# Optimization experiments

Measured on AMD Instinct MI355X. Metric: run time of the kernel, lower is better.

The kernel has to match this reference:

```python
import jax, jax.numpy as jnp
import numpy as np

N_NODES = 100000
N_EDGES = 3200000
IN_F, HID, N_CLS = 512, 16, 7


def setup_inputs() -> dict:
    key = jax.random.key(0)
    k1, k2, k3, k4 = jax.random.split(key, 4)
    x = jax.random.normal(k1, (N_NODES, IN_F), dtype=jnp.float32)
    edge_index = jax.random.randint(k2, (2, N_EDGES), 0, N_NODES, dtype=jnp.int32)
    W1 = jax.random.normal(k3, (IN_F, HID), dtype=jnp.float32) * (1.0 / np.sqrt(IN_F))
    b1 = jnp.zeros((HID,), dtype=jnp.float32)
    W2 = jax.random.normal(k4, (HID, N_CLS), dtype=jnp.float32) * (1.0 / np.sqrt(HID))
    b2 = jnp.zeros((N_CLS,), dtype=jnp.float32)
    return {"x": x, "edge_index": edge_index, "W1": W1, "b1": b1, "W2": W2, "b2": b2}


def _gcn_norm(src, dst, n_nodes):
    # symmetric normalization with self-loops already included in (src, dst)
    deg = jax.ops.segment_sum(jnp.ones(dst.shape, jnp.float32), dst, num_segments=n_nodes)
    dinv = jnp.where(deg > 0, jax.lax.rsqrt(deg), 0.0)
    return dinv[src] * dinv[dst]  # [E]


def _gcn_conv(h, src, dst, norm, W, b, n_nodes):
    # transform-first (PyG GCNConv), then normalized scatter-add aggregation
    h = h @ W                                   # [N, out]
    msg = h[src] * norm[:, None]                # gather + scale, [E, out]
    out = jax.ops.segment_sum(msg, dst, num_segments=n_nodes)  # scatter-add
    return out + b


def reference(x, edge_index, W1, b1, W2, b2):
    n = x.shape[0]
    loops = jnp.arange(n, dtype=edge_index.dtype)
    src = jnp.concatenate([edge_index[0], loops])
    dst = jnp.concatenate([edge_index[1], loops])
    norm = _gcn_norm(src, dst, n)
    h = _gcn_conv(x, src, dst, norm, W1, b1, n)
    h = jax.nn.relu(h)
    out = _gcn_conv(h, src, dst, norm, W2, b2, n)
    return out
```

## Files before the change

### kernel.cpp

```cpp
#include <hip/hip_runtime.h>

#define CHUNK 8192
#define BMAX 512

typedef __attribute__((address_space(3))) unsigned int lds_u32;
typedef const __attribute__((address_space(1))) unsigned int glb_u32;

__device__ __forceinline__ void gload16(const float* g, float* l) {
    __builtin_amdgcn_global_load_lds((glb_u32*)g, (lds_u32*)l, 16, 0, 0);
}


__global__ __launch_bounds__(256) void k_coarse_hist(const int* __restrict__ dst, int E,
                                                     int* __restrict__ bc,
                                                     int* __restrict__ blockBase, int B) {
    __shared__ int cnt[BMAX];
    int t = threadIdx.x;
    cnt[t] = 0; cnt[t + 256] = 0;
    __syncthreads();
    int e0 = blockIdx.x * CHUNK;
#pragma unroll
    for (int it = 0; it < CHUNK / 256; ++it) {
        int e = e0 + it * 256 + t;
        if (e < E) atomicAdd(&cnt[dst[e] >> 8], 1);
    }
    __syncthreads();
    for (int b = t; b < B; b += 256) {
        int c = cnt[b];
        if (c > 0) blockBase[(size_t)blockIdx.x * B + b] = atomicAdd(&bc[b], c);
    }
}

__global__ void k_scan_bsums(int* bsums, int nb) {
    __shared__ int s[2][512];
    int t = threadIdx.x;
    int v = (t < nb) ? bsums[t] : 0;
    int p = 0;
    s[0][t] = v;
    __syncthreads();
    for (int off = 1; off < 512; off <<= 1) {
        s[p ^ 1][t] = s[p][t] + ((t >= off) ? s[p][t - off] : 0);
        p ^= 1;
        __syncthreads();
    }
    if (t < nb) bsums[t] = s[p][t] - v;
}


__global__ __launch_bounds__(256) void k_coarse_scatter(const int* __restrict__ src,
                                                        const int* __restrict__ dst, int E,
                                                        const int* __restrict__ bucketBase,
                                                        const int* __restrict__ blockBase, int B,
                                                        unsigned int* __restrict__ ebuf) {
    __shared__ int run[BMAX];
    int t = threadIdx.x;
    run[t] = 0; run[t + 256] = 0;
    __syncthreads();
    int e0 = blockIdx.x * CHUNK;
#pragma unroll
    for (int it = 0; it < CHUNK / 256; ++it) {
        int e = e0 + it * 256 + t;
        if (e < E) {
            int d = dst[e];
            int b = d >> 8;
            int rank = atomicAdd(&run[b], 1);
            int pos = bucketBase[b] + blockBase[(size_t)blockIdx.x * B + b] + rank;
            ebuf[pos] = ((unsigned int)(d & 255) << 24) | (unsigned int)src[e];
        }
    }
}


__global__ __launch_bounds__(256) void k_bucket_hist(const unsigned int* __restrict__ ebuf,
                                                     const int* __restrict__ bucketBase,
                                                     int E, int N, int B,
                                                     int* __restrict__ hist,
                                                     float* __restrict__ dinv) {
    __shared__ int cnt[256];
    int t = threadIdx.x;
    int b = blockIdx.x;
    cnt[t] = 0;
    __syncthreads();
    int e0 = bucketBase[b];
    int e1 = (b + 1 < B) ? bucketBase[b + 1] : E;
    for (int e = e0 + t; e < e1; e += 256) atomicAdd(&cnt[ebuf[e] >> 24], 1);
    __syncthreads();
    int node = b * 256 + t;
    if (node < N) {
        hist[node] = cnt[t];
        dinv[node] = rsqrtf((float)(cnt[t] + 1));
    }
}


__global__ __launch_bounds__(256) void k_fine_scatter(const unsigned int* __restrict__ ebuf,
                                                      const int* __restrict__ bucketBase,
                                                      const int* __restrict__ hist,
                                                      int E, int N, int B,
                                                      int* __restrict__ rowStart,
                                                      int* __restrict__ csr_src) {
    __shared__ int s[2][256];
    __shared__ int cnt[256];
    int t = threadIdx.x;
    int b = blockIdx.x;
    int node = b * 256 + t;
    int v = (node < N) ? hist[node] : 0;
    int p = 0;
    s[0][t] = v;
    __syncthreads();
    for (int off = 1; off < 256; off <<= 1) {
        s[p ^ 1][t] = s[p][t] + ((t >= off) ? s[p][t - off] : 0);
        p ^= 1;
        __syncthreads();
    }
    int rs = bucketBase[b] + s[p][t] - v;
    if (node < N) rowStart[node] = rs;
    cnt[t] = rs;
    __syncthreads();
    int e0 = bucketBase[b];
    int e1 = (b + 1 < B) ? bucketBase[b + 1] : E;
    for (int e = e0 + t; e < e1; e += 256) {
        unsigned int w = ebuf[e];
        int pos = atomicAdd(&cnt[w >> 24], 1);
        csr_src[pos] = (int)(w & 0xFFFFFFu);
    }
}


__global__ __launch_bounds__(256) void k_gemm1(const float* __restrict__ x,
                                               const float* __restrict__ W1,
                                               const float* __restrict__ dinv,
                                               int N, float* __restrict__ h1) {
    __shared__ float xs[2][256 * 32];
    const int t = threadIdx.x;
    const int R0 = blockIdx.x * 256;
    const int tk = t & 7;

    const float* gbase[8];
#pragma unroll
    for (int it = 0; it < 8; ++it) {
        int r = it * 32 + (t >> 3);
        int j4 = tk ^ (r & 7);
        int row = R0 + r;
        if (row >= N) row = N - 1;
        gbase[it] = x + (size_t)row * 512 + j4 * 4;
    }

    float acc[16];
#pragma unroll
    for (int c = 0; c < 16; ++c) acc[c] = 0.0f;

#pragma unroll
    for (int it = 0; it < 8; ++it)
        gload16(gbase[it], &xs[0][(it * 256 + t) * 4]);
    __syncthreads();

    int p = 0;
    for (int ch = 0; ch < 16; ++ch) {
        if (ch + 1 < 16) {
#pragma unroll
            for (int it = 0; it < 8; ++it)
                gload16(gbase[it] + (ch + 1) * 32, &xs[p ^ 1][(it * 256 + t) * 4]);
        }
        const float* xr = &xs[p][t * 32];
#pragma unroll
        for (int j4 = 0; j4 < 8; ++j4) {
            float4 xv = *(const float4*)(xr + ((j4 ^ tk) << 2));
            float xe[4] = {xv.x, xv.y, xv.z, xv.w};
            int k = ch * 32 + j4 * 4;
#pragma unroll
            for (int d = 0; d < 4; ++d) {
                const float* w = W1 + (k + d) * 16;
#pragma unroll
                for (int c = 0; c < 16; ++c) acc[c] = fmaf(xe[d], w[c], acc[c]);
            }
        }
        __syncthreads();
        p ^= 1;
    }

    int row = R0 + t;
    if (row < N) {
        float di = dinv[row];
#pragma unroll
        for (int c = 0; c < 16; ++c) acc[c] *= di;
        float4* o = (float4*)(h1 + (size_t)row * 16);
        o[0] = make_float4(acc[0], acc[1], acc[2], acc[3]);
        o[1] = make_float4(acc[4], acc[5], acc[6], acc[7]);
        o[2] = make_float4(acc[8], acc[9], acc[10], acc[11]);
        o[3] = make_float4(acc[12], acc[13], acc[14], acc[15]);
    }
}


__global__ void k_gather1(const float* __restrict__ h1, const int* __restrict__ csr_src,
                          const int* __restrict__ rowStart, const int* __restrict__ hist,
                          const float* __restrict__ dinv, const float* __restrict__ b1,
                          int N, float* __restrict__ relu1) {
    int g = blockIdx.x * blockDim.x + threadIdx.x;
    int i = g >> 4, c = g & 15;
    if (i >= N) return;
    float ssum = h1[(size_t)i * 16 + c];
    int e0 = rowStart[i], e1 = e0 + hist[i];
    for (int e = e0; e < e1; ++e) {
        int s = csr_src[e];
        ssum += h1[(size_t)s * 16 + c];
    }
    float v = fmaf(dinv[i], ssum, b1[c]);
    relu1[(size_t)i * 16 + c] = fmaxf(v, 0.0f);
}


__global__ void k_h2(const float* __restrict__ relu1, const float* __restrict__ W2,
                     const float* __restrict__ dinv, int N, float* __restrict__ h2) {
    int i = blockIdx.x * blockDim.x + threadIdx.x;
    if (i >= N) return;
    float r[16];
#pragma unroll
    for (int q = 0; q < 4; ++q) {
        float4 v = *(const float4*)(relu1 + (size_t)i * 16 + q * 4);
        r[q * 4 + 0] = v.x; r[q * 4 + 1] = v.y; r[q * 4 + 2] = v.z; r[q * 4 + 3] = v.w;
    }
    float di = dinv[i];
#pragma unroll
    for (int c2 = 0; c2 < 7; ++c2) {
        float a = 0.0f;
#pragma unroll
        for (int c = 0; c < 16; ++c) a = fmaf(r[c], W2[c * 7 + c2], a);
        h2[(size_t)i * 7 + c2] = a * di;
    }
}


__global__ void k_gather2(const float* __restrict__ h2, const int* __restrict__ csr_src,
                          const int* __restrict__ rowStart, const int* __restrict__ hist,
                          const float* __restrict__ dinv, const float* __restrict__ b2,
                          int N, float* __restrict__ out) {
    int g = blockIdx.x * blockDim.x + threadIdx.x;
    int i = g >> 3, c = g & 7;
    if (i >= N || c >= 7) return;
    float ssum = h2[(size_t)i * 7 + c];
    int e0 = rowStart[i], e1 = e0 + hist[i];
    for (int e = e0; e < e1; ++e) {
        int s = csr_src[e];
        ssum += h2[(size_t)s * 7 + c];
    }
    out[(size_t)i * 7 + c] = fmaf(dinv[i], ssum, b2[c]);
}


extern "C" void kernel_launch(void* const* d_in, const int* in_sizes, int n_in,
                              void* d_out, int out_size, void* d_ws, size_t ws_size,
                              hipStream_t stream) {
    const float* x  = (const float*)d_in[0];
    const int*   ei = (const int*)d_in[1];
    const float* W1 = (const float*)d_in[2];
    const float* b1 = (const float*)d_in[3];
    const float* W2 = (const float*)d_in[4];
    const float* b2 = (const float*)d_in[5];
    float* out = (float*)d_out;

    const int N = in_sizes[0] / 512;
    const int E = in_sizes[1] / 2;
    const int* src = ei;
    const int* dst = ei + E;

    const int nb  = (N + 255) / 256;
    const int B   = nb;
    const int nbA = (E + CHUNK - 1) / CHUNK;

    char* ws = (char*)d_ws;
    auto alloc = [&](size_t bytes) {
        char* p = ws;
        ws += (bytes + 511) & ~(size_t)511;
        return p;
    };
    int*   hist      = (int*)alloc((size_t)N * 4);
    float* dinv      = (float*)alloc((size_t)N * 4);
    int*   rowStart  = (int*)alloc((size_t)N * 4);
    int*   bc        = (int*)alloc((size_t)(B + 1) * 4);
    int*   blockBase = (int*)alloc((size_t)nbA * B * 4);
    int*   csr_src   = (int*)alloc((size_t)E * 4);
    size_t featBytes = (size_t)N * 16 * 4 * 2 + (size_t)N * 7 * 4;
    size_t ebufBytes = (size_t)E * 4;
    char* regB = alloc(featBytes > ebufBytes ? featBytes : ebufBytes);
    unsigned int* ebuf = (unsigned int*)regB;
    float* h1    = (float*)regB;
    float* relu1 = h1 + (size_t)N * 16;
    float* h2    = relu1 + (size_t)N * 16;

    hipMemsetAsync(bc, 0, (size_t)B * 4, stream);
    k_coarse_hist<<<nbA, 256, 0, stream>>>(dst, E, bc, blockBase, B);
    k_scan_bsums<<<1, 512, 0, stream>>>(bc, B);
    k_coarse_scatter<<<nbA, 256, 0, stream>>>(src, dst, E, bc, blockBase, B, ebuf);
    k_bucket_hist<<<B, 256, 0, stream>>>(ebuf, bc, E, N, B, hist, dinv);
    k_fine_scatter<<<B, 256, 0, stream>>>(ebuf, bc, hist, E, N, B, rowStart, csr_src);
    k_gemm1<<<nb, 256, 0, stream>>>(x, W1, dinv, N, h1);
    k_gather1<<<(N * 16 + 255) / 256, 256, 0, stream>>>(h1, csr_src, rowStart, hist, dinv, b1, N, relu1);
    k_h2<<<nb, 256, 0, stream>>>(relu1, W2, dinv, N, h2);
    k_gather2<<<(N * 8 + 255) / 256, 256, 0, stream>>>(h2, csr_src, rowStart, hist, dinv, b2, N, out);
}
```

Before: 582.6 us.

## Split GEMM1 K-dimension across waves with LDS reduction, 64 rows per block

Rewrites the first-layer GEMM so each block handles 64 rows instead of 256. The whole 64x512 tile is loaded into LDS at once, and each of the four waves computes partial sums over a quarter of K. The partials are then reduced through LDS before dinv scaling and the store. This launches four times more blocks to raise parallelism and occupancy across CUs and removes the chunked double-buffer loop. In exchange it gives up copy/compute overlap within a block, uses 128KB LDS per block (likely one block per CU), and adds a reduction step.

Measured after the change: 604.4 us. +3.8%, slower.

```diff
diff --git a/kernel.cpp b/kernel.cpp
--- a/kernel.cpp
+++ b/kernel.cpp
@@ -131,64 +131,63 @@
                                                const float* __restrict__ W1,
                                                const float* __restrict__ dinv,
                                                int N, float* __restrict__ h1) {
-    __shared__ float xs[2][256 * 32];
+    __shared__ float xs[64 * 512];
     const int t = threadIdx.x;
-    const int R0 = blockIdx.x * 256;
-    const int tk = t & 7;
-
-    const float* gbase[8];
-#pragma unroll
-    for (int it = 0; it < 8; ++it) {
-        int r = it * 32 + (t >> 3);
-        int j4 = tk ^ (r & 7);
+    const int lane = t & 63;
+    const int w = __builtin_amdgcn_readfirstlane(t >> 6);
+    const int R0 = blockIdx.x * 64;
+
+#pragma unroll
+    for (int u = 0; u < 32; ++u) {
+        int r = w * 16 + (u >> 1);
+        int h = u & 1;
         int row = R0 + r;
         if (row >= N) row = N - 1;
-        gbase[it] = x + (size_t)row * 512 + j4 * 4;
-    }
+        const float* src = x + (size_t)row * 512 + h * 256 + ((lane ^ (r & 7)) << 2);
+        gload16(src, &xs[r * 512 + h * 256]);
+    }
+    __syncthreads();
 
     float acc[16];
 #pragma unroll
     for (int c = 0; c < 16; ++c) acc[c] = 0.0f;
-
-#pragma unroll
-    for (int it = 0; it < 8; ++it)
-        gload16(gbase[it], &xs[0][(it * 256 + t) * 4]);
-    __syncthreads();
-
-    int p = 0;
-    for (int ch = 0; ch < 16; ++ch) {
-        if (ch + 1 < 16) {
-#pragma unroll
-            for (int it = 0; it < 8; ++it)
-                gload16(gbase[it] + (ch + 1) * 32, &xs[p ^ 1][(it * 256 + t) * 4]);
+    const int sw = lane & 7;
+#pragma unroll 4
+    for (int k4 = 0; k4 < 32; ++k4) {
+        int g = w * 32 + k4;
+        const float4 xv = *(const float4*)&xs[lane * 512 + ((g ^ sw) << 2)];
+        float xe[4] = {xv.x, xv.y, xv.z, xv.w};
+        int k = g << 2;
+#pragma unroll
+        for (int d = 0; d < 4; ++d) {
+            const float* wp = W1 + (k + d) * 16;
+#pragma unroll
+            for (int c = 0; c < 16; ++c) acc[c] = fmaf(xe[d], wp[c], acc[c]);
         }
-        const float* xr = &xs[p][t * 32];
-#pragma unroll
-        for (int j4 = 0; j4 < 8; ++j4) {
-            float4 xv = *(const float4*)(xr + ((j4 ^ tk) << 2));
-            float xe[4] = {xv.x, xv.y, xv.z, xv.w};
-            int k = ch * 32 + j4 * 4;
-#pragma unroll
-            for (int d = 0; d < 4; ++d) {
-                const float* w = W1 + (k + d) * 16;
-#pragma unroll
-                for (int c = 0; c < 16; ++c) acc[c] = fmaf(xe[d], w[c], acc[c]);
-            }
-        }
-        __syncthreads();
-        p ^= 1;
-    }
-
-    int row = R0 + t;
+    }
+    __syncthreads();
+
+    float* red = xs;
+#pragma unroll
+    for (int cg = 0; cg < 4; ++cg)
+        *(float4*)&red[(w * 64 + lane) * 16 + cg * 4] =
+            make_float4(acc[cg * 4], acc[cg * 4 + 1], acc[cg * 4 + 2], acc[cg * 4 + 3]);
+    __syncthreads();
+
+    int r = t >> 2, cg = (t & 3) * 4;
+    int row = R0 + r;
     if (row < N) {
+        float4 s0 = *(float4*)&red[(0 * 64 + r) * 16 + cg];
+        float4 s1 = *(float4*)&red[(1 * 64 + r) * 16 + cg];
+        float4 s2 = *(float4*)&red[(2 * 64 + r) * 16 + cg];
+        float4 s3 = *(float4*)&red[(3 * 64 + r) * 16 + cg];
         float di = dinv[row];
-#pragma unroll
-        for (int c = 0; c < 16; ++c) acc[c] *= di;
-        float4* o = (float4*)(h1 + (size_t)row * 16);
-        o[0] = make_float4(acc[0], acc[1], acc[2], acc[3]);
-        o[1] = make_float4(acc[4], acc[5], acc[6], acc[7]);
-        o[2] = make_float4(acc[8], acc[9], acc[10], acc[11]);
-        o[3] = make_float4(acc[12], acc[13], acc[14], acc[15]);
+        float4 o;
+        o.x = (s0.x + s1.x + s2.x + s3.x) * di;
+        o.y = (s0.y + s1.y + s2.y + s3.y) * di;
+        o.z = (s0.z + s1.z + s2.z + s3.z) * di;
+        o.w = (s0.w + s1.w + s2.w + s3.w) * di;
+        *(float4*)(h1 + (size_t)row * 16 + cg) = o;
     }
 }
 
@@ -268,6 +267,7 @@
     const int nb  = (N + 255) / 256;
     const int B   = nb;
     const int nbA = (E + CHUNK - 1) / CHUNK;
+    const int nb64 = (N + 63) / 64;
 
     char* ws = (char*)d_ws;
     auto alloc = [&](size_t bytes) {
@@ -295,7 +295,7 @@
     k_coarse_scatter<<<nbA, 256, 0, stream>>>(src, dst, E, bc, blockBase, B, ebuf);
     k_bucket_hist<<<B, 256, 0, stream>>>(ebuf, bc, E, N, B, hist, dinv);
     k_fine_scatter<<<B, 256, 0, stream>>>(ebuf, bc, hist, E, N, B, rowStart, csr_src);
-    k_gemm1<<<nb, 256, 0, stream>>>(x, W1, dinv, N, h1);
+    k_gemm1<<<nb64, 256, 0, stream>>>(x, W1, dinv, N, h1);
     k_gather1<<<(N * 16 + 255) / 256, 256, 0, stream>>>(h1, csr_src, rowStart, hist, dinv, b1, N, relu1);
     k_h2<<<nb, 256, 0, stream>>>(relu1, W2, dinv, N, h2);
     k_gather2<<<(N * 8 + 255) / 256, 256, 0, stream>>>(h2, csr_src, rowStart, hist, dinv, b2, N, out);
```

## Split gemm1 output columns across waves with 64-row blocks for occupancy

Applied to the files above, without the earlier changes.

The first-layer GEMM now processes 64 rows per block instead of 256. Each of the four waves computes a 4-column slice of the 16 outputs for all 64 rows, so a thread holds 4 accumulators instead of 16. LDS shrinks from 64KB to 16KB, and launch bounds request 6 blocks per CU, with the aim of more occupancy and more blocks to hide the latency of streaming x. In exchange, each x element in LDS is read by four waves instead of one, and W1 is read four times per row.

New measurement: 558.7 us. -4.1%, faster.

```diff
diff --git a/kernel.cpp b/kernel.cpp
--- a/kernel.cpp
+++ b/kernel.cpp
@@ -127,68 +127,65 @@
 }
 
 
-__global__ __launch_bounds__(256) void k_gemm1(const float* __restrict__ x,
-                                               const float* __restrict__ W1,
-                                               const float* __restrict__ dinv,
-                                               int N, float* __restrict__ h1) {
-    __shared__ float xs[2][256 * 32];
+__global__ __launch_bounds__(256, 6) void k_gemm1(const float* __restrict__ x,
+                                                  const float* __restrict__ W1,
+                                                  const float* __restrict__ dinv,
+                                                  int N, float* __restrict__ h1) {
+    __shared__ float xs[2][2048];
     const int t = threadIdx.x;
-    const int R0 = blockIdx.x * 256;
-    const int tk = t & 7;
-
-    const float* gbase[8];
-#pragma unroll
-    for (int it = 0; it < 8; ++it) {
-        int r = it * 32 + (t >> 3);
-        int j4 = tk ^ (r & 7);
+    const int lane = t & 63;
+    const int cq = __builtin_amdgcn_readfirstlane(t >> 6);
+    const int R0 = blockIdx.x * 64;
+
+    const float* gbase[2];
+#pragma unroll
+    for (int u = 0; u < 2; ++u) {
+        int r = (cq * 2 + u) * 8 + (lane >> 3);
+        int g = lane & 7;
         int row = R0 + r;
         if (row >= N) row = N - 1;
-        gbase[it] = x + (size_t)row * 512 + j4 * 4;
-    }
-
-    float acc[16];
-#pragma unroll
-    for (int c = 0; c < 16; ++c) acc[c] = 0.0f;
-
-#pragma unroll
-    for (int it = 0; it < 8; ++it)
-        gload16(gbase[it], &xs[0][(it * 256 + t) * 4]);
-    __syncthreads();
-
+        gbase[u] = x + (size_t)row * 512 + ((g ^ (r & 7)) << 2);
+    }
+
+    float acc[4] = {0.f, 0.f, 0.f, 0.f};
+
+#pragma unroll
+    for (int u = 0; u < 2; ++u)
+        gload16(gbase[u], &xs[0][((cq * 2 + u) * 64 + lane) * 4]);
+    __syncthreads();
+
+    const int row = lane;
+    const int rs = row & 7;
     int p = 0;
     for (int ch = 0; ch < 16; ++ch) {
         if (ch + 1 < 16) {
 #pragma unroll
-            for (int it = 0; it < 8; ++it)
-                gload16(gbase[it] + (ch + 1) * 32, &xs[p ^ 1][(it * 256 + t) * 4]);
+            for (int u = 0; u < 2; ++u)
+                gload16(gbase[u] + (ch + 1) * 32, &xs[p ^ 1][((cq * 2 + u) * 64 + lane) * 4]);
         }
-        const float* xr = &xs[p][t * 32];
-#pragma unroll
-        for (int j4 = 0; j4 < 8; ++j4) {
-            float4 xv = *(const float4*)(xr + ((j4 ^ tk) << 2));
+        const float* xr = &xs[p][row * 32];
+#pragma unroll
+        for (int j = 0; j < 8; ++j) {
+            int j4 = (j + cq * 2) & 7;
+            float4 xv = *(const float4*)(xr + ((j4 ^ rs) << 2));
             float xe[4] = {xv.x, xv.y, xv.z, xv.w};
             int k = ch * 32 + j4 * 4;
 #pragma unroll
             for (int d = 0; d < 4; ++d) {
-                const float* w = W1 + (k + d) * 16;
-#pragma unroll
-                for (int c = 0; c < 16; ++c) acc[c] = fmaf(xe[d], w[c], acc[c]);
+                const float* wp = W1 + (k + d) * 16 + cq * 4;
+#pragma unroll
+                for (int c = 0; c < 4; ++c) acc[c] = fmaf(xe[d], wp[c], acc[c]);
             }
         }
         __syncthreads();
         p ^= 1;
     }
 
-    int row = R0 + t;
-    if (row < N) {
-        float di = dinv[row];
-#pragma unroll
-        for (int c = 0; c < 16; ++c) acc[c] *= di;
-        float4* o = (float4*)(h1 + (size_t)row * 16);
-        o[0] = make_float4(acc[0], acc[1], acc[2], acc[3]);
-        o[1] = make_float4(acc[4], acc[5], acc[6], acc[7]);
-        o[2] = make_float4(acc[8], acc[9], acc[10], acc[11]);
-        o[3] = make_float4(acc[12], acc[13], acc[14], acc[15]);
+    int orow = R0 + row;
+    if (orow < N) {
+        float di = dinv[orow];
+        *(float4*)(h1 + (size_t)orow * 16 + cq * 4) =
+            make_float4(acc[0] * di, acc[1] * di, acc[2] * di, acc[3] * di);
     }
 }
 
@@ -268,6 +265,7 @@
     const int nb  = (N + 255) / 256;
     const int B   = nb;
     const int nbA = (E + CHUNK - 1) / CHUNK;
+    const int nb64 = (N + 63) / 64;
 
     char* ws = (char*)d_ws;
     auto alloc = [&](size_t bytes) {
@@ -295,7 +293,7 @@
     k_coarse_scatter<<<nbA, 256, 0, stream>>>(src, dst, E, bc, blockBase, B, ebuf);
     k_bucket_hist<<<B, 256, 0, stream>>>(ebuf, bc, E, N, B, hist, dinv);
     k_fine_scatter<<<B, 256, 0, stream>>>(ebuf, bc, hist, E, N, B, rowStart, csr_src);
-    k_gemm1<<<nb, 256, 0, stream>>>(x, W1, dinv, N, h1);
+    k_gemm1<<<nb64, 256, 0, stream>>>(x, W1, dinv, N, h1);
     k_gather1<<<(N * 16 + 255) / 256, 256, 0, stream>>>(h1, csr_src, rowStart, hist, dinv, b1, N, relu1);
     k_h2<<<nb, 256, 0, stream>>>(relu1, W2, dinv, N, h2);
     k_gather2<<<(N * 8 + 255) / 256, 256, 0, stream>>>(h2, csr_src, rowStart, hist, dinv, b2, N, out);
```
